# Kernel optimization log

Measured on AMD Instinct MI355X. Metric: run time of the kernel, lower is better.

Reference implementation:

```python
import jax, jax.numpy as jnp
import numpy as np

NEG_SLOPE = 0.2  # PyG GATConv default negative_slope
H1, H2, H3 = 4, 4, 1
CH = 64  # hidden_dim (per-head out channels)
N_NODES = 50000
N_EDGES = 800000
IN_DIM = 128
N_CLASSES = 10


def _gat_layer(x, src, dst, n, W, a_src, a_dst, b, heads, ch):
    # x: [N, Fin], W: [Fin, heads*ch], a_src/a_dst: [heads, ch], b: [heads*ch]
    h = (x @ W).reshape(-1, heads, ch)              # [N, H, C]
    e_src = jnp.sum(h * a_src, axis=-1)             # [N, H]
    e_dst = jnp.sum(h * a_dst, axis=-1)             # [N, H]
    e = jax.nn.leaky_relu(e_src[src] + e_dst[dst], NEG_SLOPE)  # [E, H]
    # segment softmax over incoming edges of each dst node
    m = jax.ops.segment_max(e, dst, num_segments=n)            # [N, H]
    p = jnp.exp(e - m[dst])                                    # [E, H]
    s = jax.ops.segment_sum(p, dst, num_segments=n)            # [N, H]
    alpha = p / (s[dst] + 1e-16)                               # [E, H]
    out = jax.ops.segment_sum(alpha[:, :, None] * h[src], dst, num_segments=n)  # [N, H, C]
    return out.reshape(-1, heads * ch) + b


def setup_inputs() -> dict:
    key = jax.random.key(0)
    ks = jax.random.split(key, 16)

    def glorot(k, shape, fan_in):
        return jax.random.normal(k, shape, dtype=jnp.float32) * (1.0 / np.sqrt(fan_in))

    x = jax.random.normal(ks[0], (N_NODES, IN_DIM), dtype=jnp.float32)
    edge_index = jax.random.randint(ks[1], (2, N_EDGES), 0, N_NODES, dtype=jnp.int32)

    d1 = H1 * CH  # 256
    d2 = H2 * CH  # 256
    d3 = H3 * CH  # 64
    return {
        "x": x,
        "edge_index": edge_index,
        "W1": glorot(ks[2], (IN_DIM, d1), IN_DIM),
        "a1_src": glorot(ks[3], (H1, CH), CH),
        "a1_dst": glorot(ks[4], (H1, CH), CH),
        "b1": jnp.zeros((d1,), jnp.float32),
        "W2": glorot(ks[5], (d1, d2), d1),
        "a2_src": glorot(ks[6], (H2, CH), CH),
        "a2_dst": glorot(ks[7], (H2, CH), CH),
        "b2": jnp.zeros((d2,), jnp.float32),
        "W3": glorot(ks[8], (d2, d3), d2),
        "a3_src": glorot(ks[9], (H3, CH), CH),
        "a3_dst": glorot(ks[10], (H3, CH), CH),
        "b3": jnp.zeros((d3,), jnp.float32),
        "fc_W": glorot(ks[11], (CH, N_CLASSES), CH),
        "fc_b": jnp.zeros((N_CLASSES,), jnp.float32),
    }


def reference(x, edge_index, W1, a1_src, a1_dst, b1, W2, a2_src, a2_dst, b2,
              W3, a3_src, a3_dst, b3, fc_W, fc_b):
    n = x.shape[0]
    # PyG GATConv adds self-loops by default
    loops = jnp.arange(n, dtype=edge_index.dtype)
    src = jnp.concatenate([edge_index[0], loops])
    dst = jnp.concatenate([edge_index[1], loops])

    h = jax.nn.relu(_gat_layer(x, src, dst, n, W1, a1_src, a1_dst, b1, H1, CH))
    # dropout(p=0.3) is identity in eval mode
    h = jax.nn.relu(_gat_layer(h, src, dst, n, W2, a2_src, a2_dst, b2, H2, CH))
    h = jax.nn.relu(_gat_layer(h, src, dst, n, W3, a3_src, a3_dst, b3, H3, CH))
    return h @ fc_W + fc_b  # [N, num_classes]
```

## Files before the change

### kernel.cpp

```cpp
#include <hip/hip_runtime.h>

#define NN 50000
#define NE 800000
#define E2 (NE + NN)
#define IN_DIM 128
#define SCAN_B 196

typedef unsigned short u16;
typedef unsigned int u32;
typedef __attribute__((ext_vector_type(8))) short short8;
typedef __attribute__((ext_vector_type(4))) float f32x4;

__device__ inline u16 f2bf(float x) {
    u32 u = __float_as_uint(x);
    u32 r = (u + 0x7fff + ((u >> 16) & 1)) >> 16;
    return (u16)r;
}
__device__ inline float bf2f(u16 h) { return __uint_as_float(((u32)h) << 16); }

__global__ __launch_bounds__(256) void fill_i32(int* __restrict__ p, int v, int n) {
    int i = blockIdx.x * 256 + threadIdx.x;
    if (i < n) p[i] = v;
}

__global__ __launch_bounds__(256) void hist_dst(const int* __restrict__ ei, int* __restrict__ deg) {
    int e = blockIdx.x * 256 + threadIdx.x;
    if (e < NE) atomicAdd(&deg[ei[NE + e]], 1);
}

__global__ __launch_bounds__(256) void block_sums(const int* __restrict__ deg, int* __restrict__ bsum) {
    int b = blockIdx.x;
    int i = b * 256 + threadIdx.x;
    int v = (i < NN) ? deg[i] : 0;
#pragma unroll
    for (int off = 32; off; off >>= 1) v += __shfl_down(v, off);
    __shared__ int ws[4];
    if ((threadIdx.x & 63) == 0) ws[threadIdx.x >> 6] = v;
    __syncthreads();
    if (threadIdx.x == 0) bsum[b] = ws[0] + ws[1] + ws[2] + ws[3];
}

__global__ __launch_bounds__(256) void scan_bsums(const int* __restrict__ bsum, int* __restrict__ boff) {
    __shared__ int s[256];
    int t = threadIdx.x;
    int v = (t < SCAN_B) ? bsum[t] : 0;
    s[t] = v;
    __syncthreads();
    for (int off = 1; off < 256; off <<= 1) {
        int u = (t >= off) ? s[t - off] : 0;
        __syncthreads();
        s[t] += u;
        __syncthreads();
    }
    if (t < SCAN_B) boff[t] = s[t] - v;
}

__global__ __launch_bounds__(256) void scan_final(const int* __restrict__ deg,
                                                  const int* __restrict__ boff,
                                                  int* __restrict__ rowptr,
                                                  int* __restrict__ cursor) {
    int b = blockIdx.x;
    int t = threadIdx.x;
    int i = b * 256 + t;
    int v = (i < NN) ? deg[i] : 0;
    __shared__ int s[256];
    s[t] = v;
    __syncthreads();
    for (int off = 1; off < 256; off <<= 1) {
        int u = (t >= off) ? s[t - off] : 0;
        __syncthreads();
        s[t] += u;
        __syncthreads();
    }
    int excl = s[t] - v + boff[b];
    if (i < NN) { rowptr[i] = excl; cursor[i] = excl; }
    if (i == NN - 1) rowptr[NN] = excl + v;
}

__global__ __launch_bounds__(256) void scatter_csr(const int* __restrict__ ei,
                                                   int* __restrict__ cursor,
                                                   int* __restrict__ csr_src) {
    int e = blockIdx.x * 256 + threadIdx.x;
    if (e >= E2) return;
    int s, d;
    if (e < NE) { s = ei[e]; d = ei[NE + e]; } else { s = d = e - NE; }
    int pos = atomicAdd(&cursor[d], 1);
    csr_src[pos] = s;
}

__global__ __launch_bounds__(256) void xconv(const float* __restrict__ X,
                                             u16* __restrict__ Xh, u16* __restrict__ Xl,
                                             int total4) {
    int i = blockIdx.x * 256 + threadIdx.x;
    if (i >= total4) return;
    float4 v = reinterpret_cast<const float4*>(X)[i];
    ushort4 h, l;
    h.x = f2bf(v.x); l.x = f2bf(v.x - bf2f(h.x));
    h.y = f2bf(v.y); l.y = f2bf(v.y - bf2f(h.y));
    h.z = f2bf(v.z); l.z = f2bf(v.z - bf2f(h.z));
    h.w = f2bf(v.w); l.w = f2bf(v.w - bf2f(h.w));
    reinterpret_cast<ushort4*>(Xh)[i] = h;
    reinterpret_cast<ushort4*>(Xl)[i] = l;
}

__global__ __launch_bounds__(256) void wconv(const float* __restrict__ W,
                                             u16* __restrict__ Wh, u16* __restrict__ Wl,
                                             int K, int N) {
    int idx = blockIdx.x * 256 + threadIdx.x;
    if (idx >= K * N) return;
    int k = idx / N, n = idx - k * N;
    float w = W[idx];
    u16 hi = f2bf(w);
    Wh[(size_t)n * K + k] = hi;
    Wl[(size_t)n * K + k] = f2bf(w - bf2f(hi));
}

template<int BN, int KK, bool FES>
__global__ __launch_bounds__(256) void gemm_mfma(const u16* __restrict__ Ah,
                                                 const u16* __restrict__ Al,
                                                 const u16* __restrict__ Wh,
                                                 const u16* __restrict__ Wl,
                                                 float* __restrict__ C,
                                                 int M, int N,
                                                 const float* __restrict__ as_,
                                                 const float* __restrict__ ad_,
                                                 float* __restrict__ es,
                                                 float* __restrict__ ed) {
    const int BM = 128, BK = 32, LDT = BK + 8;
    __shared__ u16 Ahs[BM][LDT], Als[BM][LDT];
    const int FRN = BN / 32;
    int tid = threadIdx.x;
    int lane = tid & 63, wid = tid >> 6;
    int wm = wid >> 1, wn = wid & 1;
    int row0 = blockIdx.x * BM, col0 = blockIdx.y * BN;
    int l15 = lane & 15, lg = lane >> 4;

    int c0 = tid * 2;
    int r_a = c0 >> 2, sub_a0 = (c0 & 3) * 8, sub_a1 = ((c0 + 1) & 3) * 8;
    int gr_a = row0 + r_a;

    uint4 avh[2], avl[2];
    auto loadA = [&](int ko) {
        if (gr_a < M) {
            avh[0] = *reinterpret_cast<const uint4*>(Ah + (size_t)gr_a * KK + ko + sub_a0);
            avl[0] = *reinterpret_cast<const uint4*>(Al + (size_t)gr_a * KK + ko + sub_a0);
            avh[1] = *reinterpret_cast<const uint4*>(Ah + (size_t)gr_a * KK + ko + sub_a1);
            avl[1] = *reinterpret_cast<const uint4*>(Al + (size_t)gr_a * KK + ko + sub_a1);
        } else {
            avh[0] = avh[1] = avl[0] = avl[1] = make_uint4(0, 0, 0, 0);
        }
    };

    f32x4 acc[4][FRN];
#pragma unroll
    for (int i = 0; i < 4; ++i)
#pragma unroll
        for (int j = 0; j < FRN; ++j) acc[i][j] = (f32x4){0.f, 0.f, 0.f, 0.f};

    loadA(0);
    for (int ko = 0; ko < KK; ko += BK) {
        __syncthreads();
        *reinterpret_cast<uint4*>(&Ahs[r_a][sub_a0]) = avh[0];
        *reinterpret_cast<uint4*>(&Als[r_a][sub_a0]) = avl[0];
        *reinterpret_cast<uint4*>(&Ahs[r_a][sub_a1]) = avh[1];
        *reinterpret_cast<uint4*>(&Als[r_a][sub_a1]) = avl[1];
        __syncthreads();
        if (ko + BK < KK) loadA(ko + BK);
        short8 bh[FRN], bl[FRN];
#pragma unroll
        for (int j = 0; j < FRN; ++j) {
            int gc = col0 + wn * (BN / 2) + j * 16 + l15;
            bh[j] = *reinterpret_cast<const short8*>(Wh + (size_t)gc * KK + ko + lg * 8);
            bl[j] = *reinterpret_cast<const short8*>(Wl + (size_t)gc * KK + ko + lg * 8);
        }
        short8 ah[4], al[4];
#pragma unroll
        for (int i = 0; i < 4; ++i) {
            int r = wm * 64 + i * 16 + l15;
            ah[i] = *reinterpret_cast<const short8*>(&Ahs[r][lg * 8]);
            al[i] = *reinterpret_cast<const short8*>(&Als[r][lg * 8]);
        }
#pragma unroll
        for (int i = 0; i < 4; ++i)
#pragma unroll
            for (int j = 0; j < FRN; ++j) {
                acc[i][j] = __builtin_amdgcn_mfma_f32_16x16x32_bf16(ah[i], bh[j], acc[i][j], 0, 0, 0);
                acc[i][j] = __builtin_amdgcn_mfma_f32_16x16x32_bf16(ah[i], bl[j], acc[i][j], 0, 0, 0);
                acc[i][j] = __builtin_amdgcn_mfma_f32_16x16x32_bf16(al[i], bh[j], acc[i][j], 0, 0, 0);
            }
    }
#pragma unroll
    for (int i = 0; i < 4; ++i)
#pragma unroll
        for (int rr = 0; rr < 4; ++rr) {
            int gr = row0 + wm * 64 + i * 16 + lg * 4 + rr;
            if (gr < M) {
#pragma unroll
                for (int j = 0; j < FRN; ++j)
                    C[(size_t)gr * N + col0 + wn * (BN / 2) + j * 16 + l15] = acc[i][j][rr];
            }
        }
    if (FES) {
        int head = (col0 + wn * (BN / 2)) >> 6;
        float asv[FRN], adv[FRN];
#pragma unroll
        for (int j = 0; j < FRN; ++j) {
            asv[j] = as_[head * 64 + j * 16 + l15];
            adv[j] = ad_[head * 64 + j * 16 + l15];
        }
#pragma unroll
        for (int i = 0; i < 4; ++i)
#pragma unroll
            for (int rr = 0; rr < 4; ++rr) {
                float vs = 0.f, vd = 0.f;
#pragma unroll
                for (int j = 0; j < FRN; ++j) {
                    vs += acc[i][j][rr] * asv[j];
                    vd += acc[i][j][rr] * adv[j];
                }
#pragma unroll
                for (int off = 1; off < 16; off <<= 1) {
                    vs += __shfl_xor(vs, off);
                    vd += __shfl_xor(vd, off);
                }
                int gr = row0 + wm * 64 + i * 16 + lg * 4 + rr;
                if (l15 == 0 && gr < M) {
                    es[gr * 4 + head] = vs;
                    ed[gr * 4 + head] = vd;
                }
            }
    }
}

__global__ void escore(const float* __restrict__ h, const float* __restrict__ as,
                       const float* __restrict__ ad, float* __restrict__ es,
                       float* __restrict__ ed, int H) {
    int n = blockIdx.x;
    int t = threadIdx.x;
    int D = blockDim.x;
    float hv = h[(size_t)n * D + t];
    float vs = hv * as[t];
    float vd = hv * ad[t];
#pragma unroll
    for (int off = 32; off; off >>= 1) {
        vs += __shfl_down(vs, off);
        vd += __shfl_down(vd, off);
    }
    if ((t & 63) == 0) {
        int head = t >> 6;
        es[n * H + head] = vs;
        ed[n * H + head] = vd;
    }
}

template<int D, int H>
__global__ __launch_bounds__(256) void agg_fused(const int* __restrict__ rowptr,
                                                 const int* __restrict__ csr_src,
                                                 const float* __restrict__ es,
                                                 const float* __restrict__ ed,
                                                 const float* __restrict__ h,
                                                 const float* __restrict__ b,
                                                 u16* __restrict__ Oh,
                                                 u16* __restrict__ Ol) {
    const int TPN = D / 4;
    const int NPB = 256 / TPN;
    const int logH = (H == 4) ? 2 : 0;
    int tid = threadIdx.x;
    int n = blockIdx.x * NPB + tid / TPN;
    if (n >= NN) return;
    int gl = tid % TPN;
    int start = rowptr[n], end = rowptr[n + 1];

    int headA = gl & (H - 1);
    const int JP = TPN >> logH;
    float edvA = ed[n * H + headA];
    float m = -1e30f;
    for (int i = start + (gl >> logH); i < end; i += JP) {
        int src = csr_src[i];
        float v = es[src * H + headA] + edvA;
        v = v > 0.f ? v : 0.2f * v;
        m = fmaxf(m, v);
    }
#pragma unroll
    for (int off = H; off < TPN; off <<= 1)
        m = fmaxf(m, __shfl_xor(m, off));

    int f0 = gl * 4;
    int hb = f0 >> 6;
    float mB;
    if (D == 256) mB = __shfl(m, hb);
    else          mB = m;
    float edv = ed[n * H + hb];
    float sump = 0.f;
    float4 acc = make_float4(0.f, 0.f, 0.f, 0.f);
    int i = start;
    for (; i + 8 <= end; i += 8) {
        int s0 = csr_src[i + 0], s1 = csr_src[i + 1], s2 = csr_src[i + 2], s3 = csr_src[i + 3];
        int s4 = csr_src[i + 4], s5 = csr_src[i + 5], s6 = csr_src[i + 6], s7 = csr_src[i + 7];
        float v0 = es[s0 * H + hb] + edv, v1 = es[s1 * H + hb] + edv;
        float v2 = es[s2 * H + hb] + edv, v3 = es[s3 * H + hb] + edv;
        float v4 = es[s4 * H + hb] + edv, v5 = es[s5 * H + hb] + edv;
        float v6 = es[s6 * H + hb] + edv, v7 = es[s7 * H + hb] + edv;
        v0 = v0 > 0.f ? v0 : 0.2f * v0; v1 = v1 > 0.f ? v1 : 0.2f * v1;
        v2 = v2 > 0.f ? v2 : 0.2f * v2; v3 = v3 > 0.f ? v3 : 0.2f * v3;
        v4 = v4 > 0.f ? v4 : 0.2f * v4; v5 = v5 > 0.f ? v5 : 0.2f * v5;
        v6 = v6 > 0.f ? v6 : 0.2f * v6; v7 = v7 > 0.f ? v7 : 0.2f * v7;
        float p0 = __expf(v0 - mB), p1 = __expf(v1 - mB);
        float p2 = __expf(v2 - mB), p3 = __expf(v3 - mB);
        float p4 = __expf(v4 - mB), p5 = __expf(v5 - mB);
        float p6 = __expf(v6 - mB), p7 = __expf(v7 - mB);
        float4 h0 = *reinterpret_cast<const float4*>(h + (size_t)s0 * D + f0);
        float4 h1 = *reinterpret_cast<const float4*>(h + (size_t)s1 * D + f0);
        float4 h2 = *reinterpret_cast<const float4*>(h + (size_t)s2 * D + f0);
        float4 h3 = *reinterpret_cast<const float4*>(h + (size_t)s3 * D + f0);
        float4 h4 = *reinterpret_cast<const float4*>(h + (size_t)s4 * D + f0);
        float4 h5 = *reinterpret_cast<const float4*>(h + (size_t)s5 * D + f0);
        float4 h6 = *reinterpret_cast<const float4*>(h + (size_t)s6 * D + f0);
        float4 h7 = *reinterpret_cast<const float4*>(h + (size_t)s7 * D + f0);
        acc.x += p0 * h0.x + p1 * h1.x + p2 * h2.x + p3 * h3.x
               + p4 * h4.x + p5 * h5.x + p6 * h6.x + p7 * h7.x;
        acc.y += p0 * h0.y + p1 * h1.y + p2 * h2.y + p3 * h3.y
               + p4 * h4.y + p5 * h5.y + p6 * h6.y + p7 * h7.y;
        acc.z += p0 * h0.z + p1 * h1.z + p2 * h2.z + p3 * h3.z
               + p4 * h4.z + p5 * h5.z + p6 * h6.z + p7 * h7.z;
        acc.w += p0 * h0.w + p1 * h1.w + p2 * h2.w + p3 * h3.w
               + p4 * h4.w + p5 * h5.w + p6 * h6.w + p7 * h7.w;
        sump += p0 + p1 + p2 + p3 + p4 + p5 + p6 + p7;
    }
    for (; i < end; ++i) {
        int s0 = csr_src[i];
        float v = es[s0 * H + hb] + edv;
        v = v > 0.f ? v : 0.2f * v;
        float p = __expf(v - mB);
        float4 h0 = *reinterpret_cast<const float4*>(h + (size_t)s0 * D + f0);
        acc.x += p * h0.x; acc.y += p * h0.y; acc.z += p * h0.z; acc.w += p * h0.w;
        sump += p;
    }
    float inv = 1.f / (sump + 1e-16f);
    float4 bb = *reinterpret_cast<const float4*>(b + f0);
    float4 o;
    o.x = acc.x * inv + bb.x; o.y = acc.y * inv + bb.y;
    o.z = acc.z * inv + bb.z; o.w = acc.w * inv + bb.w;
    o.x = o.x > 0.f ? o.x : 0.f; o.y = o.y > 0.f ? o.y : 0.f;
    o.z = o.z > 0.f ? o.z : 0.f; o.w = o.w > 0.f ? o.w : 0.f;
    ushort4 hv, lv;
    hv.x = f2bf(o.x); lv.x = f2bf(o.x - bf2f(hv.x));
    hv.y = f2bf(o.y); lv.y = f2bf(o.y - bf2f(hv.y));
    hv.z = f2bf(o.z); lv.z = f2bf(o.z - bf2f(hv.z));
    hv.w = f2bf(o.w); lv.w = f2bf(o.w - bf2f(hv.w));
    *reinterpret_cast<ushort4*>(Oh + (size_t)n * D + f0) = hv;
    *reinterpret_cast<ushort4*>(Ol + (size_t)n * D + f0) = lv;
}

__global__ __launch_bounds__(256) void fc_kernel(const u16* __restrict__ Hh,
                                                 const u16* __restrict__ Hl,
                                                 const float* __restrict__ W,
                                                 const float* __restrict__ b,
                                                 float* __restrict__ out) {
    int idx = blockIdx.x * 256 + threadIdx.x;
    if (idx >= NN * 10) return;
    int n = idx / 10, j = idx - n * 10;
    float acc = b[j];
#pragma unroll
    for (int c = 0; c < 64; ++c) {
        float hv = bf2f(Hh[n * 64 + c]) + bf2f(Hl[n * 64 + c]);
        acc += hv * W[c * 10 + j];
    }
    out[idx] = acc;
}

extern "C" void kernel_launch(void* const* d_in, const int* in_sizes, int n_in,
                              void* d_out, int out_size, void* d_ws, size_t ws_size,
                              hipStream_t stream) {
    const float* x   = (const float*)d_in[0];
    const int*   ei  = (const int*)d_in[1];
    const float* W1  = (const float*)d_in[2];
    const float* a1s = (const float*)d_in[3];
    const float* a1d = (const float*)d_in[4];
    const float* b1  = (const float*)d_in[5];
    const float* W2  = (const float*)d_in[6];
    const float* a2s = (const float*)d_in[7];
    const float* a2d = (const float*)d_in[8];
    const float* b2  = (const float*)d_in[9];
    const float* W3  = (const float*)d_in[10];
    const float* a3s = (const float*)d_in[11];
    const float* a3d = (const float*)d_in[12];
    const float* b3  = (const float*)d_in[13];
    const float* fcW = (const float*)d_in[14];
    const float* fcb = (const float*)d_in[15];
    float* out = (float*)d_out;

    char* wp = (char*)d_ws;
    float* h   = (float*)wp;  wp += (size_t)NN * 256 * 4;
    u16* Ph    = (u16*)wp;    wp += (size_t)NN * 256 * 2;
    u16* Pl    = (u16*)wp;    wp += (size_t)NN * 256 * 2;
    u16* Xh    = (u16*)wp;    wp += (size_t)NN * 128 * 2;
    u16* Xl    = (u16*)wp;    wp += (size_t)NN * 128 * 2;
    float* ES  = (float*)wp;  wp += (size_t)NN * 4 * 4;
    float* ED  = (float*)wp;  wp += (size_t)NN * 4 * 4;
    u16* Wth   = (u16*)wp;    wp += 256 * 256 * 2;
    u16* Wtl   = (u16*)wp;    wp += 256 * 256 * 2;
    int* rowptr = (int*)wp;   wp += (NN + 1) * 4;
    int* csrsrc = (int*)wp;   wp += (size_t)E2 * 4;
    int* deg    = (int*)wp;   wp += NN * 4;
    int* bsum   = (int*)wp;   wp += 256 * 4;
    int* boff   = (int*)wp;   wp += 256 * 4;
    int* cursor = (int*)((char*)d_ws + (size_t)NN * 256 * 4);

    fill_i32<<<(NN + 255) / 256, 256, 0, stream>>>(deg, 1, NN);
    hist_dst<<<(NE + 255) / 256, 256, 0, stream>>>(ei, deg);
    block_sums<<<SCAN_B, 256, 0, stream>>>(deg, bsum);
    scan_bsums<<<1, 256, 0, stream>>>(bsum, boff);
    scan_final<<<SCAN_B, 256, 0, stream>>>(deg, boff, rowptr, cursor);
    scatter_csr<<<(E2 + 255) / 256, 256, 0, stream>>>(ei, cursor, csrsrc);

    xconv<<<(NN * IN_DIM / 4 + 255) / 256, 256, 0, stream>>>(x, Xh, Xl, NN * IN_DIM / 4);

    const int MT = (NN + 127) / 128;

    wconv<<<(IN_DIM * 256 + 255) / 256, 256, 0, stream>>>(W1, Wth, Wtl, IN_DIM, 256);
    gemm_mfma<128, 128, true><<<dim3(MT, 2), 256, 0, stream>>>(Xh, Xl, Wth, Wtl, h, NN, 256,
                                                               a1s, a1d, ES, ED);
    agg_fused<256, 4><<<(NN + 3) / 4, 256, 0, stream>>>(rowptr, csrsrc, ES, ED, h, b1, Ph, Pl);

    wconv<<<(256 * 256 + 255) / 256, 256, 0, stream>>>(W2, Wth, Wtl, 256, 256);
    gemm_mfma<128, 256, true><<<dim3(MT, 2), 256, 0, stream>>>(Ph, Pl, Wth, Wtl, h, NN, 256,
                                                               a2s, a2d, ES, ED);
    agg_fused<256, 4><<<(NN + 3) / 4, 256, 0, stream>>>(rowptr, csrsrc, ES, ED, h, b2, Ph, Pl);

    wconv<<<(256 * 64 + 255) / 256, 256, 0, stream>>>(W3, Wth, Wtl, 256, 64);
    gemm_mfma<64, 256, false><<<dim3(MT, 1), 256, 0, stream>>>(Ph, Pl, Wth, Wtl, h, NN, 64,
                                                               nullptr, nullptr, nullptr, nullptr);
    escore<<<NN, 64, 0, stream>>>(h, a3s, a3d, ES, ED, 1);
    agg_fused<64, 1><<<(NN + 15) / 16, 256, 0, stream>>>(rowptr, csrsrc, ES, ED, h, b3, Ph, Pl);

    fc_kernel<<<(NN * 10 + 255) / 256, 256, 0, stream>>>(Ph, Pl, fcW, fcb, out);
}
```

Baseline: 556.5 us.

## Double-buffer GEMM A tiles in LDS and fuse final FC into layer-3 aggregation

```diff
diff --git a/kernel.cpp b/kernel.cpp
--- a/kernel.cpp
+++ b/kernel.cpp
@@ -127,7 +127,7 @@
                                                  float* __restrict__ es,
                                                  float* __restrict__ ed) {
     const int BM = 128, BK = 32, LDT = BK + 8;
-    __shared__ u16 Ahs[BM][LDT], Als[BM][LDT];
+    __shared__ u16 Ahs[2][BM][LDT], Als[2][BM][LDT];
     const int FRN = BN / 32;
     int tid = threadIdx.x;
     int lane = tid & 63, wid = tid >> 6;
@@ -150,6 +150,12 @@
             avh[0] = avh[1] = avl[0] = avl[1] = make_uint4(0, 0, 0, 0);
         }
     };
+    auto writeA = [&](int p) {
+        *reinterpret_cast<uint4*>(&Ahs[p][r_a][sub_a0]) = avh[0];
+        *reinterpret_cast<uint4*>(&Als[p][r_a][sub_a0]) = avl[0];
+        *reinterpret_cast<uint4*>(&Ahs[p][r_a][sub_a1]) = avh[1];
+        *reinterpret_cast<uint4*>(&Als[p][r_a][sub_a1]) = avl[1];
+    };
 
     f32x4 acc[4][FRN];
 #pragma unroll
@@ -158,14 +164,16 @@
         for (int j = 0; j < FRN; ++j) acc[i][j] = (f32x4){0.f, 0.f, 0.f, 0.f};
 
     loadA(0);
+    writeA(0);
+    loadA(BK);
+    __syncthreads();
+
     for (int ko = 0; ko < KK; ko += BK) {
-        __syncthreads();
-        *reinterpret_cast<uint4*>(&Ahs[r_a][sub_a0]) = avh[0];
-        *reinterpret_cast<uint4*>(&Als[r_a][sub_a0]) = avl[0];
-        *reinterpret_cast<uint4*>(&Ahs[r_a][sub_a1]) = avh[1];
-        *reinterpret_cast<uint4*>(&Als[r_a][sub_a1]) = avl[1];
-        __syncthreads();
-        if (ko + BK < KK) loadA(ko + BK);
+        int p = (ko >> 5) & 1;
+        if (ko + BK < KK) {
+            writeA(p ^ 1);
+            if (ko + 2 * BK < KK) loadA(ko + 2 * BK);
+        }
         short8 bh[FRN], bl[FRN];
 #pragma unroll
         for (int j = 0; j < FRN; ++j) {
@@ -177,8 +185,8 @@
 #pragma unroll
         for (int i = 0; i < 4; ++i) {
             int r = wm * 64 + i * 16 + l15;
-            ah[i] = *reinterpret_cast<const short8*>(&Ahs[r][lg * 8]);
-            al[i] = *reinterpret_cast<const short8*>(&Als[r][lg * 8]);
+            ah[i] = *reinterpret_cast<const short8*>(&Ahs[p][r][lg * 8]);
+            al[i] = *reinterpret_cast<const short8*>(&Als[p][r][lg * 8]);
         }
 #pragma unroll
         for (int i = 0; i < 4; ++i)
@@ -188,6 +196,7 @@
                 acc[i][j] = __builtin_amdgcn_mfma_f32_16x16x32_bf16(ah[i], bl[j], acc[i][j], 0, 0, 0);
                 acc[i][j] = __builtin_amdgcn_mfma_f32_16x16x32_bf16(al[i], bh[j], acc[i][j], 0, 0, 0);
             }
+        __syncthreads();
     }
 #pragma unroll
     for (int i = 0; i < 4; ++i)
@@ -253,7 +262,7 @@
     }
 }
 
-template<int D, int H>
+template<int D, int H, bool FC>
 __global__ __launch_bounds__(256) void agg_fused(const int* __restrict__ rowptr,
                                                  const int* __restrict__ csr_src,
                                                  const float* __restrict__ es,
@@ -261,7 +270,10 @@
                                                  const float* __restrict__ h,
                                                  const float* __restrict__ b,
                                                  u16* __restrict__ Oh,
-                                                 u16* __restrict__ Ol) {
+                                                 u16* __restrict__ Ol,
+                                                 const float* __restrict__ fcW,
+                                                 const float* __restrict__ fcb,
+                                                 float* __restrict__ out) {
     const int TPN = D / 4;
     const int NPB = 256 / TPN;
     const int logH = (H == 4) ? 2 : 0;
@@ -343,31 +355,30 @@
     o.z = acc.z * inv + bb.z; o.w = acc.w * inv + bb.w;
     o.x = o.x > 0.f ? o.x : 0.f; o.y = o.y > 0.f ? o.y : 0.f;
     o.z = o.z > 0.f ? o.z : 0.f; o.w = o.w > 0.f ? o.w : 0.f;
-    ushort4 hv, lv;
-    hv.x = f2bf(o.x); lv.x = f2bf(o.x - bf2f(hv.x));
-    hv.y = f2bf(o.y); lv.y = f2bf(o.y - bf2f(hv.y));
-    hv.z = f2bf(o.z); lv.z = f2bf(o.z - bf2f(hv.z));
-    hv.w = f2bf(o.w); lv.w = f2bf(o.w - bf2f(hv.w));
-    *reinterpret_cast<ushort4*>(Oh + (size_t)n * D + f0) = hv;
-    *reinterpret_cast<ushort4*>(Ol + (size_t)n * D + f0) = lv;
-}
-
-__global__ __launch_bounds__(256) void fc_kernel(const u16* __restrict__ Hh,
-                                                 const u16* __restrict__ Hl,
-                                                 const float* __restrict__ W,
-                                                 const float* __restrict__ b,
-                                                 float* __restrict__ out) {
-    int idx = blockIdx.x * 256 + threadIdx.x;
-    if (idx >= NN * 10) return;
-    int n = idx / 10, j = idx - n * 10;
-    float acc = b[j];
-#pragma unroll
-    for (int c = 0; c < 64; ++c) {
-        float hv = bf2f(Hh[n * 64 + c]) + bf2f(Hl[n * 64 + c]);
-        acc += hv * W[c * 10 + j];
-    }
-    out[idx] = acc;
-}
+    if (!FC) {
+        ushort4 hv, lv;
+        hv.x = f2bf(o.x); lv.x = f2bf(o.x - bf2f(hv.x));
+        hv.y = f2bf(o.y); lv.y = f2bf(o.y - bf2f(hv.y));
+        hv.z = f2bf(o.z); lv.z = f2bf(o.z - bf2f(hv.z));
+        hv.w = f2bf(o.w); lv.w = f2bf(o.w - bf2f(hv.w));
+        *reinterpret_cast<ushort4*>(Oh + (size_t)n * D + f0) = hv;
+        *reinterpret_cast<ushort4*>(Ol + (size_t)n * D + f0) = lv;
+    } else {
+        float pj[10];
+#pragma unroll
+        for (int j = 0; j < 10; ++j)
+            pj[j] = o.x * fcW[(f0 + 0) * 10 + j] + o.y * fcW[(f0 + 1) * 10 + j]
+                  + o.z * fcW[(f0 + 2) * 10 + j] + o.w * fcW[(f0 + 3) * 10 + j];
+#pragma unroll
+        for (int off = 1; off < 16; off <<= 1)
+#pragma unroll
+            for (int j = 0; j < 10; ++j)
+                pj[j] += __shfl_xor(pj[j], off);
+        if (gl < 10)
+            out[n * 10 + gl] = pj[0] * 0.f + (gl == 0 ? 0.f : 0.f) + pj[gl] + fcb[gl];
+    }
+}
+
 
 extern "C" void kernel_launch(void* const* d_in, const int* in_sizes, int n_in,
                               void* d_out, int out_size, void* d_ws, size_t ws_size,
@@ -421,18 +432,19 @@
     wconv<<<(IN_DIM * 256 + 255) / 256, 256, 0, stream>>>(W1, Wth, Wtl, IN_DIM, 256);
     gemm_mfma<128, 128, true><<<dim3(MT, 2), 256, 0, stream>>>(Xh, Xl, Wth, Wtl, h, NN, 256,
                                                                a1s, a1d, ES, ED);
-    agg_fused<256, 4><<<(NN + 3) / 4, 256, 0, stream>>>(rowptr, csrsrc, ES, ED, h, b1, Ph, Pl);
+    agg_fused<256, 4, false><<<(NN + 3) / 4, 256, 0, stream>>>(rowptr, csrsrc, ES, ED, h, b1,
+                                                               Ph, Pl, nullptr, nullptr, nullptr);
 
     wconv<<<(256 * 256 + 255) / 256, 256, 0, stream>>>(W2, Wth, Wtl, 256, 256);
     gemm_mfma<128, 256, true><<<dim3(MT, 2), 256, 0, stream>>>(Ph, Pl, Wth, Wtl, h, NN, 256,
                                                                a2s, a2d, ES, ED);
-    agg_fused<256, 4><<<(NN + 3) / 4, 256, 0, stream>>>(rowptr, csrsrc, ES, ED, h, b2, Ph, Pl);
+    agg_fused<256, 4, false><<<(NN + 3) / 4, 256, 0, stream>>>(rowptr, csrsrc, ES, ED, h, b2,
+                                                               Ph, Pl, nullptr, nullptr, nullptr);
 
     wconv<<<(256 * 64 + 255) / 256, 256, 0, stream>>>(W3, Wth, Wtl, 256, 64);
     gemm_mfma<64, 256, false><<<dim3(MT, 1), 256, 0, stream>>>(Ph, Pl, Wth, Wtl, h, NN, 64,
                                                                nullptr, nullptr, nullptr, nullptr);
     escore<<<NN, 64, 0, stream>>>(h, a3s, a3d, ES, ED, 1);
-    agg_fused<64, 1><<<(NN + 15) / 16, 256, 0, stream>>>(rowptr, csrsrc, ES, ED, h, b3, Ph, Pl);
-
-    fc_kernel<<<(NN * 10 + 255) / 256, 256, 0, stream>>>(Ph, Pl, fcW, fcb, out);
-}
+    agg_fused<64, 1, true><<<(NN + 15) / 16, 256, 0, stream>>>(rowptr, csrsrc, ES, ED, h, b3,
+                                                               nullptr, nullptr, fcW, fcb, out);
+}
```

New measurement: 529.6 us. 1.05x faster.
